# Optimization experiments

Hardware: AMD Instinct MI355X
Metric: run time of the kernel (lower is better)

Reference implementation:

```python
import jax, jax.numpy as jnp
import numpy as np

D_MODEL = 2048
N_HEADS = 16
HEAD_DIM = D_MODEL // N_HEADS  # 128
B, S = 2, 2048


def setup_inputs() -> dict:
    key = jax.random.key(0)
    k1, k2, k3, k4 = jax.random.split(key, 4)
    scale = 0.02
    X = jax.random.normal(k1, (B, S, D_MODEL), dtype=jnp.float32)
    Wq = jax.random.normal(k2, (D_MODEL, D_MODEL), dtype=jnp.float32) * scale
    Wkv = jax.random.normal(k3, (2 * HEAD_DIM, D_MODEL), dtype=jnp.float32) * scale
    Wo = jax.random.normal(k4, (D_MODEL, D_MODEL), dtype=jnp.float32) * scale
    return {"X": X, "Wq": Wq, "Wkv": Wkv, "Wo": Wo}


def reference(X, Wq, Wkv, Wo):
    Bt, St, Dm = X.shape
    # Q: [B, H, S, hd]
    Q = (X @ Wq.T).reshape(Bt, St, N_HEADS, HEAD_DIM).transpose(0, 2, 1, 3)
    # Shared single-head K/V: [B, S, hd] each (no materialized head broadcast)
    KV = X @ Wkv.T
    K, V = KV[..., :HEAD_DIM], KV[..., HEAD_DIM:]
    # Scores: [B, H, S, S]; K shared across heads via einsum broadcast
    scores = jnp.einsum("bhqd,bkd->bhqk", Q, K) / jnp.sqrt(jnp.float32(HEAD_DIM))
    causal = jnp.tril(jnp.ones((St, St), dtype=bool))
    scores = jnp.where(causal[None, None], scores, jnp.finfo(scores.dtype).min)
    attn = jax.nn.softmax(scores, axis=-1)
    heads = jnp.einsum("bhqk,bkd->bhqd", attn, V)  # [B, H, S, hd]
    concat = heads.transpose(0, 2, 1, 3).reshape(Bt, St, Dm)
    return concat @ Wo.T
```

## Files before the change

### kernel.cpp

```cpp
#include <hip/hip_runtime.h>
#include <hip/hip_bf16.h>
#include <stdint.h>

#define DM 2048
#define NH 16
#define HD 128
#define NB 2
#define SQ 2048

typedef __bf16 bf16x8 __attribute__((ext_vector_type(8)));
typedef float f32x4 __attribute__((ext_vector_type(4)));

typedef __attribute__((address_space(1))) uint32_t as1_u32;
typedef __attribute__((address_space(3))) uint32_t as3_u32;

__device__ __forceinline__ void gload16(const void* g, void* l) {
  __builtin_amdgcn_global_load_lds((const as1_u32*)g, (as3_u32*)l, 16, 0, 0);
}

__device__ __forceinline__ unsigned short f2bf(float f) {
  __hip_bfloat16 h = __float2bfloat16(f);
  return __builtin_bit_cast(unsigned short, h);
}

__device__ __forceinline__ int swz(int r) { return (r ^ (r >> 3)) & 7; }

__global__ void cast_f32_to_bf16(const float* __restrict__ in,
                                 unsigned short* __restrict__ out, int n) {
  int stride = gridDim.x * blockDim.x * 4;
  for (int i = (blockIdx.x * blockDim.x + threadIdx.x) * 4; i < n; i += stride) {
    float4 v = *reinterpret_cast<const float4*>(in + i);
    ushort4 o;
    o.x = f2bf(v.x); o.y = f2bf(v.y); o.z = f2bf(v.z); o.w = f2bf(v.w);
    *reinterpret_cast<ushort4*>(out + i) = o;
  }
}

__global__ void cast_weights(const float* __restrict__ Wq,
                             const float* __restrict__ Wkv,
                             const float* __restrict__ Wo,
                             unsigned short* __restrict__ Wqkvb,
                             unsigned short* __restrict__ Wob) {
  const int n = 4194304 + 524288 + 4194304;
  int stride = gridDim.x * blockDim.x * 4;
  for (int i = (blockIdx.x * blockDim.x + threadIdx.x) * 4; i < n; i += stride) {
    const float* src; unsigned short* dst;
    if (i < 4194304)      { src = Wq + i;            dst = Wqkvb + i; }
    else if (i < 4718592) { src = Wkv + (i - 4194304); dst = Wqkvb + i; }
    else                  { src = Wo + (i - 4718592);  dst = Wob + (i - 4718592); }
    float4 v = *reinterpret_cast<const float4*>(src);
    ushort4 o;
    o.x = f2bf(v.x); o.y = f2bf(v.y); o.z = f2bf(v.z); o.w = f2bf(v.w);
    *reinterpret_cast<ushort4*>(dst) = o;
  }
}

template<int MODE>
__global__ void gemm_bt(const unsigned short* __restrict__ A,
                        const unsigned short* __restrict__ Bm,
                        void* __restrict__ C0, void* __restrict__ C1,
                        void* __restrict__ C2,
                        int M, int N, int K, float scale) {
  __shared__ unsigned short As[128 * 32];
  __shared__ unsigned short Bs[128 * 32];
  const int t = threadIdx.x;
  const int w = t >> 6, l = t & 63;
  const int lr = l & 15, lkb = (l >> 4) * 8;
  const int m0 = blockIdx.x * 128, n0 = blockIdx.y * 128;
  const int wr = (w >> 1) * 64, wc = (w & 1) * 64;
  f32x4 acc[4][4] = {};
  for (int k0 = 0; k0 < K; k0 += 32) {
#pragma unroll
    for (int p = 0; p < 2; ++p) {
      int seg = p * 256 + t;
      int row = seg >> 2, c8 = (seg & 3) * 8;
      gload16(A + (size_t)(m0 + row) * K + k0 + c8, (void*)(As + seg * 8));
      gload16(Bm + (size_t)(n0 + row) * K + k0 + c8, (void*)(Bs + seg * 8));
    }
    __syncthreads();
    bf16x8 af[4], bfv[4];
#pragma unroll
    for (int mi = 0; mi < 4; ++mi)
      af[mi] = *reinterpret_cast<const bf16x8*>(As + (wr + mi * 16 + lr) * 32 + lkb);
#pragma unroll
    for (int ni = 0; ni < 4; ++ni)
      bfv[ni] = *reinterpret_cast<const bf16x8*>(Bs + (wc + ni * 16 + lr) * 32 + lkb);
#pragma unroll
    for (int mi = 0; mi < 4; ++mi)
#pragma unroll
      for (int ni = 0; ni < 4; ++ni)
        acc[mi][ni] = __builtin_amdgcn_mfma_f32_16x16x32_bf16(af[mi], bfv[ni], acc[mi][ni], 0, 0, 0);
    __syncthreads();
  }
#pragma unroll
  for (int mi = 0; mi < 4; ++mi) {
#pragma unroll
    for (int ni = 0; ni < 4; ++ni) {
      const int r0 = m0 + wr + mi * 16 + (l >> 4) * 4;
      const int cc = n0 + wc + ni * 16 + lr;
#pragma unroll
      for (int j = 0; j < 4; ++j) {
        float v = acc[mi][ni][j];
        if (MODE == 1) {
          ((float*)C0)[(size_t)(r0 + j) * N + cc] = v;
        } else {
          int m = r0 + j;
          if (cc < DM) {
            ((unsigned short*)C0)[(size_t)m * DM + cc] = f2bf(v * scale);
          } else if (cc < DM + HD) {
            ((unsigned short*)C1)[(size_t)m * HD + (cc - DM)] = f2bf(v);
          } else {
            int b = m >> 11, s = m & (SQ - 1);
            int c = s & 127;
            int sp = (s & ~127) + ((c & 15) * 8 + (c >> 4));
            ((unsigned short*)C2)[((size_t)b * HD + (cc - DM - HD)) * SQ + sp] = f2bf(v);
          }
        }
      }
    }
  }
}

__global__ __launch_bounds__(256) void mqa_attn(const unsigned short* __restrict__ Qb,
                                                const unsigned short* __restrict__ Kc,
                                                const unsigned short* __restrict__ Vt,
                                                unsigned short* __restrict__ Hb) {
  __shared__ unsigned short Ks[128 * 128];
  __shared__ unsigned short Vs[128 * 128];
  const int t = threadIdx.x, w = t >> 6, l = t & 63;
  const int lr = l & 15, hi = l >> 4;
  const int lkb = hi * 8;
  const int id = blockIdx.x;
  const int pp = id & 255;
  const int bh = pp >> 3, k8 = pp & 7;
  const int qt = (id < 256) ? (15 - k8) : k8;
  const int b = bh >> 4, h = bh & 15;
  const int q0 = qt * 128;

  bf16x8 qf[2][4];
#pragma unroll
  for (int mi = 0; mi < 2; ++mi)
#pragma unroll
    for (int kk = 0; kk < 4; ++kk) {
      const uint4* p = reinterpret_cast<const uint4*>(
          Qb + (size_t)(b * SQ + q0 + w * 32 + mi * 16 + lr) * DM + h * HD + kk * 32 + lkb);
      qf[mi][kk] = __builtin_bit_cast(bf16x8, *p);
    }
  f32x4 o[2][8] = {};
  float mrun[2][4], lrun[2][4];
#pragma unroll
  for (int mi = 0; mi < 2; ++mi)
#pragma unroll
    for (int j = 0; j < 4; ++j) { mrun[mi][j] = -3.0e38f; lrun[mi][j] = 0.f; }

  for (int kt = 0; kt <= qt; ++kt) {
    const unsigned short* Kg = Kc + (size_t)(b * SQ + kt * 128) * HD;
    const unsigned short* Vg = Vt + (size_t)b * HD * SQ + kt * 128;
#pragma unroll
    for (int p = 0; p < 8; ++p) {
      int seg = p * 256 + t;
      int row = seg >> 4, sl = seg & 15;
      int slx = sl ^ swz(row);
      gload16(Kg + (size_t)row * HD + slx * 8, (void*)(Ks + seg * 8));
      gload16(Vg + (size_t)row * SQ + slx * 8, (void*)(Vs + seg * 8));
    }
    __syncthreads();

    f32x4 s[2][8] = {};
#pragma unroll
    for (int kk = 0; kk < 4; ++kk) {
      bf16x8 kf[8];
#pragma unroll
      for (int ni = 0; ni < 8; ++ni) {
        int r = ni * 16 + lr;
        kf[ni] = *reinterpret_cast<const bf16x8*>(
            Ks + r * 128 + (((kk * 4 + hi) ^ swz(r)) << 3));
      }
#pragma unroll
      for (int mi = 0; mi < 2; ++mi)
#pragma unroll
        for (int ni = 0; ni < 8; ++ni)
          s[mi][ni] = __builtin_amdgcn_mfma_f32_16x16x32_bf16(qf[mi][kk], kf[ni], s[mi][ni], 0, 0, 0);
    }

    if (kt == qt) {
#pragma unroll
      for (int mi = 0; mi < 2; ++mi)
#pragma unroll
        for (int ni = 0; ni < 8; ++ni)
#pragma unroll
          for (int j = 0; j < 4; ++j) {
            int rq = w * 32 + mi * 16 + hi * 4 + j;
            int ck = ni * 16 + lr;
            if (ck > rq) s[mi][ni][j] = -3.0e38f;
          }
    }

#pragma unroll
    for (int mi = 0; mi < 2; ++mi) {
#pragma unroll
      for (int j = 0; j < 4; ++j) {
        float pm = s[mi][0][j];
#pragma unroll
        for (int ni = 1; ni < 8; ++ni) pm = fmaxf(pm, s[mi][ni][j]);
#pragma unroll
        for (int dd = 1; dd < 16; dd <<= 1) pm = fmaxf(pm, __shfl_xor(pm, dd));
        if (pm > mrun[mi][j]) {
          float sc = __expf(mrun[mi][j] - pm);
          mrun[mi][j] = pm;
          lrun[mi][j] *= sc;
#pragma unroll
          for (int ni = 0; ni < 8; ++ni) o[mi][ni][j] *= sc;
        }
        float mnew = mrun[mi][j];
        float rs = 0.f;
#pragma unroll
        for (int ni = 0; ni < 8; ++ni) {
          float pv = __expf(s[mi][ni][j] - mnew);
          s[mi][ni][j] = pv;
          rs += pv;
        }
#pragma unroll
        for (int dd = 1; dd < 16; dd <<= 1) rs += __shfl_xor(rs, dd);
        lrun[mi][j] += rs;
      }
    }

    __syncthreads();
    unsigned short* Ps = Ks + w * 32 * 128;
#pragma unroll
    for (int mi = 0; mi < 2; ++mi)
#pragma unroll
      for (int j = 0; j < 4; ++j) {
        int prow = mi * 16 + hi * 4 + j;
        unsigned short pk[8];
#pragma unroll
        for (int ni = 0; ni < 8; ++ni) pk[ni] = f2bf(s[mi][ni][j]);
        *reinterpret_cast<uint4*>(Ps + prow * 128 + ((lr ^ swz(prow)) << 3)) =
            *reinterpret_cast<const uint4*>(pk);
      }

#pragma unroll
    for (int kk = 0; kk < 4; ++kk) {
      bf16x8 pa[2], vf[8];
#pragma unroll
      for (int mi = 0; mi < 2; ++mi) {
        int r = mi * 16 + lr;
        pa[mi] = *reinterpret_cast<const bf16x8*>(
            Ps + r * 128 + (((kk * 4 + hi) ^ swz(r)) << 3));
      }
#pragma unroll
      for (int ni = 0; ni < 8; ++ni) {
        int r = ni * 16 + lr;
        vf[ni] = *reinterpret_cast<const bf16x8*>(
            Vs + r * 128 + (((kk * 4 + hi) ^ swz(r)) << 3));
      }
#pragma unroll
      for (int mi = 0; mi < 2; ++mi)
#pragma unroll
        for (int ni = 0; ni < 8; ++ni)
          o[mi][ni] = __builtin_amdgcn_mfma_f32_16x16x32_bf16(pa[mi], vf[ni], o[mi][ni], 0, 0, 0);
    }
    __syncthreads();
  }

#pragma unroll
  for (int mi = 0; mi < 2; ++mi)
#pragma unroll
    for (int ni = 0; ni < 8; ++ni)
#pragma unroll
      for (int j = 0; j < 4; ++j) {
        int q = q0 + w * 32 + mi * 16 + hi * 4 + j;
        float val = o[mi][ni][j] / lrun[mi][j];
        Hb[(size_t)(b * SQ + q) * DM + h * HD + ni * 16 + lr] = f2bf(val);
      }
}

extern "C" void kernel_launch(void* const* d_in, const int* in_sizes, int n_in,
                              void* d_out, int out_size, void* d_ws, size_t ws_size,
                              hipStream_t stream) {
  const float* X   = (const float*)d_in[0];
  const float* Wq  = (const float*)d_in[1];
  const float* Wkv = (const float*)d_in[2];
  const float* Wo  = (const float*)d_in[3];
  char* ws = (char*)d_ws;
  unsigned short* Xb    = (unsigned short*)(ws + 0);
  unsigned short* Wqkvb = (unsigned short*)(ws + 16777216);
  unsigned short* Wob   = (unsigned short*)(ws + 26214400);
  unsigned short* Qb    = (unsigned short*)(ws + 34603008);
  unsigned short* Kc    = (unsigned short*)(ws + 51380224);
  unsigned short* Vt    = (unsigned short*)(ws + 52428800);
  unsigned short* Hb    = (unsigned short*)(ws + 53477376);

  cast_f32_to_bf16<<<2048, 256, 0, stream>>>(X, Xb, NB * SQ * DM);
  cast_weights<<<2048, 256, 0, stream>>>(Wq, Wkv, Wo, Wqkvb, Wob);

  gemm_bt<2><<<dim3(32, 18), 256, 0, stream>>>(Xb, Wqkvb, Qb, Kc, Vt,
                                               NB * SQ, DM + 2 * HD, DM,
                                               0.08838834764831845f);
  mqa_attn<<<512, 256, 0, stream>>>(Qb, Kc, Vt, Hb);
  gemm_bt<1><<<dim3(32, 16), 256, 0, stream>>>(Hb, Wob, d_out, nullptr, nullptr,
                                               NB * SQ, DM, DM, 1.0f);
}
```

Before: 314.3 us.

## Load K/V fragments directly from global memory, skip masked diagonal MFMAs, use exp2

The attention kernel no longer stages K and V tiles through shared memory. Each wave reads its MFMA fragments straight from global memory, relying on L1/L2 because K and V are shared across heads. This drops the block-wide barriers and cuts LDS use to a per-wave P buffer, which should allow more resident blocks. On the diagonal tile, each wave skips K loads and MFMAs for column blocks that the causal mask fully removes. Softmax now uses exp2, with log2(e) folded into the Q scale. The cost is redundant global traffic across waves and exposed global-load latency in the inner loop.

Result: slower. 407.9 us (+29.8%).

```diff
diff --git a/kernel.cpp b/kernel.cpp
--- a/kernel.cpp
+++ b/kernel.cpp
@@ -125,8 +125,7 @@
                                                 const unsigned short* __restrict__ Kc,
                                                 const unsigned short* __restrict__ Vt,
                                                 unsigned short* __restrict__ Hb) {
-  __shared__ unsigned short Ks[128 * 128];
-  __shared__ unsigned short Vs[128 * 128];
+  __shared__ unsigned short Ps_all[4 * 32 * 128];
   const int t = threadIdx.x, w = t >> 6, l = t & 63;
   const int lr = l & 15, hi = l >> 4;
   const int lkb = hi * 8;
@@ -136,6 +135,7 @@
   const int qt = (id < 256) ? (15 - k8) : k8;
   const int b = bh >> 4, h = bh & 15;
   const int q0 = qt * 128;
+  unsigned short* Ps = Ps_all + w * 32 * 128;
 
   bf16x8 qf[2][4];
 #pragma unroll
@@ -154,36 +154,29 @@
     for (int j = 0; j < 4; ++j) { mrun[mi][j] = -3.0e38f; lrun[mi][j] = 0.f; }
 
   for (int kt = 0; kt <= qt; ++kt) {
+    const bool diag = (kt == qt);
+    const int nlim = diag ? 2 * w + 2 : 8;
     const unsigned short* Kg = Kc + (size_t)(b * SQ + kt * 128) * HD;
     const unsigned short* Vg = Vt + (size_t)b * HD * SQ + kt * 128;
-#pragma unroll
-    for (int p = 0; p < 8; ++p) {
-      int seg = p * 256 + t;
-      int row = seg >> 4, sl = seg & 15;
-      int slx = sl ^ swz(row);
-      gload16(Kg + (size_t)row * HD + slx * 8, (void*)(Ks + seg * 8));
-      gload16(Vg + (size_t)row * SQ + slx * 8, (void*)(Vs + seg * 8));
-    }
-    __syncthreads();
 
     f32x4 s[2][8] = {};
 #pragma unroll
     for (int kk = 0; kk < 4; ++kk) {
       bf16x8 kf[8];
 #pragma unroll
-      for (int ni = 0; ni < 8; ++ni) {
-        int r = ni * 16 + lr;
-        kf[ni] = *reinterpret_cast<const bf16x8*>(
-            Ks + r * 128 + (((kk * 4 + hi) ^ swz(r)) << 3));
-      }
+      for (int ni = 0; ni < 8; ++ni)
+        if (ni < nlim)
+          kf[ni] = __builtin_bit_cast(bf16x8, *reinterpret_cast<const uint4*>(
+              Kg + (size_t)(ni * 16 + lr) * HD + kk * 32 + lkb));
 #pragma unroll
       for (int mi = 0; mi < 2; ++mi)
 #pragma unroll
         for (int ni = 0; ni < 8; ++ni)
-          s[mi][ni] = __builtin_amdgcn_mfma_f32_16x16x32_bf16(qf[mi][kk], kf[ni], s[mi][ni], 0, 0, 0);
-    }
-
-    if (kt == qt) {
+          if (ni < nlim)
+            s[mi][ni] = __builtin_amdgcn_mfma_f32_16x16x32_bf16(qf[mi][kk], kf[ni], s[mi][ni], 0, 0, 0);
+    }
+
+    if (diag) {
 #pragma unroll
       for (int mi = 0; mi < 2; ++mi)
 #pragma unroll
@@ -206,7 +199,7 @@
 #pragma unroll
         for (int dd = 1; dd < 16; dd <<= 1) pm = fmaxf(pm, __shfl_xor(pm, dd));
         if (pm > mrun[mi][j]) {
-          float sc = __expf(mrun[mi][j] - pm);
+          float sc = __builtin_amdgcn_exp2f(mrun[mi][j] - pm);
           mrun[mi][j] = pm;
           lrun[mi][j] *= sc;
 #pragma unroll
@@ -216,7 +209,7 @@
         float rs = 0.f;
 #pragma unroll
         for (int ni = 0; ni < 8; ++ni) {
-          float pv = __expf(s[mi][ni][j] - mnew);
+          float pv = __builtin_amdgcn_exp2f(s[mi][ni][j] - mnew);
           s[mi][ni][j] = pv;
           rs += pv;
         }
@@ -226,8 +219,6 @@
       }
     }
 
-    __syncthreads();
-    unsigned short* Ps = Ks + w * 32 * 128;
 #pragma unroll
     for (int mi = 0; mi < 2; ++mi)
 #pragma unroll
@@ -243,6 +234,10 @@
 #pragma unroll
     for (int kk = 0; kk < 4; ++kk) {
       bf16x8 pa[2], vf[8];
+#pragma unroll
+      for (int ni = 0; ni < 8; ++ni)
+        vf[ni] = __builtin_bit_cast(bf16x8, *reinterpret_cast<const uint4*>(
+            Vg + (size_t)(ni * 16 + lr) * SQ + kk * 32 + lkb));
 #pragma unroll
       for (int mi = 0; mi < 2; ++mi) {
         int r = mi * 16 + lr;
@@ -250,18 +245,11 @@
             Ps + r * 128 + (((kk * 4 + hi) ^ swz(r)) << 3));
       }
 #pragma unroll
-      for (int ni = 0; ni < 8; ++ni) {
-        int r = ni * 16 + lr;
-        vf[ni] = *reinterpret_cast<const bf16x8*>(
-            Vs + r * 128 + (((kk * 4 + hi) ^ swz(r)) << 3));
-      }
-#pragma unroll
       for (int mi = 0; mi < 2; ++mi)
 #pragma unroll
         for (int ni = 0; ni < 8; ++ni)
           o[mi][ni] = __builtin_amdgcn_mfma_f32_16x16x32_bf16(pa[mi], vf[ni], o[mi][ni], 0, 0, 0);
     }
-    __syncthreads();
   }
 
 #pragma unroll
@@ -297,7 +285,7 @@
 
   gemm_bt<2><<<dim3(32, 18), 256, 0, stream>>>(Xb, Wqkvb, Qb, Kc, Vt,
                                                NB * SQ, DM + 2 * HD, DM,
-                                               0.08838834764831845f);
+                                               0.1275174293f);
   mqa_attn<<<512, 256, 0, stream>>>(Qb, Kc, Vt, Hb);
   gemm_bt<1><<<dim3(32, 16), 256, 0, stream>>>(Hb, Wob, d_out, nullptr, nullptr,
                                                NB * SQ, DM, DM, 1.0f);
```
